# Optimization experiments

Hardware: AMD Instinct MI355X
Metric: run time of the kernel (lower is better)

Reference implementation:

```python
import jax, jax.numpy as jnp
import numpy as np

LAMBDA = 0.7
K = 3
HIDDEN = 8
IN_F = 512
OUT_F = 256
N = 4096


def _gat_layer(x, adj, W, a):
    # h = fc(x); e[i,j] = attn([h_i ; h_j]) = h_i @ a[:F] + h_j @ a[F:]
    # (same math as the N*N repeat/cat/linear, without materializing [N*N, 2F])
    h = x @ W                      # [N, F]
    F_ = h.shape[1]
    src = h @ a[:F_]               # [N, 1]
    dst = h @ a[F_:]               # [N, 1]
    e = src + dst.T                # [N, N]
    att = jax.nn.softmax(e, axis=1) * adj
    return jax.nn.elu(att @ h)     # [N, F]


def setup_inputs() -> dict:
    key = jax.random.key(0)
    ks = jax.random.split(key, 8)
    x = jax.random.normal(ks[0], (N, IN_F), dtype=jnp.float32)
    # binarized sparse-ish adjacency stored densely (avg degree ~41)
    adj = (jax.random.uniform(ks[1], (N, N)) < 0.01).astype(jnp.float32)
    W1 = jax.random.normal(ks[2], (IN_F, HIDDEN), dtype=jnp.float32) * (1.0 / np.sqrt(IN_F))
    a1 = jax.random.normal(ks[3], (2 * HIDDEN, 1), dtype=jnp.float32) * (1.0 / np.sqrt(2 * HIDDEN))
    W2 = jax.random.normal(ks[4], (HIDDEN, 1), dtype=jnp.float32) * (1.0 / np.sqrt(HIDDEN))
    a2 = jax.random.normal(ks[5], (2, 1), dtype=jnp.float32)
    W_sgc = jax.random.normal(ks[6], (IN_F * K, OUT_F), dtype=jnp.float32) * (1.0 / np.sqrt(IN_F * K))
    b_sgc = jnp.zeros((OUT_F,), dtype=jnp.float32)
    return {"x": x, "adj": adj, "W1": W1, "a1": a1, "W2": W2, "a2": a2,
            "W_sgc": W_sgc, "b_sgc": b_sgc}


def reference(x, adj, W1, a1, W2, a2, W_sgc, b_sgc):
    # GAT scoring head (dropout p=0.6 is identity at inference)
    h1 = _gat_layer(x, adj, W1, a1)
    node_scores = _gat_layer(h1, adj, W2, a2)        # [N, 1]

    # K-hop adjacency powers
    adj_list = [adj]
    for _ in range(1, K):
        adj_list.append(adj_list[-1] @ adj)

    # dynamic per-row masking (row-broadcast of node_scores > lambda)
    change_mask = (node_scores > LAMBDA).astype(adj.dtype)  # [N, 1] broadcasts over cols
    for k in range(K - 1):
        adj_list[k] = adj_list[k] * change_mask
        adj_list[k + 1] = adj_list[k + 1] * (1.0 - change_mask)

    # SGC: concat K hop-aggregated features, then linear
    agg = jnp.concatenate([A @ x for A in adj_list], axis=1)  # [N, K*IN_F]
    return agg @ W_sgc + b_sgc
```

## Files before the change

### kernel.cpp

```cpp
#include <hip/hip_runtime.h>
#include <hip/hip_bf16.h>
#include <cstddef>

#define NNODE 4096
#define INF   512
#define OUTF  256
#define HID   8
#define CAP   128

typedef __attribute__((ext_vector_type(8))) short short8;
typedef __attribute__((ext_vector_type(4))) float f32x4;

__device__ __forceinline__ unsigned short f2bf(float f){
  unsigned int u = __float_as_uint(f);
  u += 0x7fffu + ((u >> 16) & 1u);
  return (unsigned short)(u >> 16);
}

__global__ __launch_bounds__(256) void build_csr(const float* __restrict__ adj,
                                                 int* __restrict__ deg,
                                                 int* __restrict__ cols){
  int row = blockIdx.x, tid = threadIdx.x;
  __shared__ int cnt;
  if (tid == 0) cnt = 0;
  __syncthreads();
  const float4* arow = (const float4*)(adj + (size_t)row * NNODE);
  int* crow = cols + (size_t)row * CAP;
  #pragma unroll
  for (int k = 0; k < 4; k++){
    int idx = k * 256 + tid;
    float4 v = arow[idx];
    int n0 = (v.x != 0.f), n1 = (v.y != 0.f), n2 = (v.z != 0.f), n3 = (v.w != 0.f);
    int m = n0 + n1 + n2 + n3;
    if (m){
      int base = atomicAdd(&cnt, m);
      int c = idx * 4;
      if (n0){ if (base < CAP) crow[base] = c;     base++; }
      if (n1){ if (base < CAP) crow[base] = c + 1; base++; }
      if (n2){ if (base < CAP) crow[base] = c + 2; base++; }
      if (n3){ if (base < CAP) crow[base] = c + 3; }
    }
  }
  __syncthreads();
  if (tid == 0) deg[row] = cnt > CAP ? CAP : cnt;
}

__global__ __launch_bounds__(256) void gat_h(const float* __restrict__ x,
                                             const float* __restrict__ W1,
                                             const float* __restrict__ a1,
                                             float* __restrict__ h,
                                             float* __restrict__ dstv){
  int wave = threadIdx.x >> 6, lane = threadIdx.x & 63;
  int row = blockIdx.x * 4 + wave;
  const float* xr = x + (size_t)row * INF;
  float acc[HID];
  #pragma unroll
  for (int f = 0; f < HID; f++) acc[f] = 0.f;
  for (int k = lane; k < INF; k += 64){
    float xv = xr[k];
    const float* wp = W1 + (size_t)k * HID;
    #pragma unroll
    for (int f = 0; f < HID; f++) acc[f] += xv * wp[f];
  }
  #pragma unroll
  for (int f = 0; f < HID; f++)
    for (int o = 32; o >= 1; o >>= 1) acc[f] += __shfl_xor(acc[f], o, 64);
  if (lane == 0){
    float d = 0.f;
    #pragma unroll
    for (int f = 0; f < HID; f++){ h[(size_t)row*HID + f] = acc[f]; d += acc[f] * a1[HID + f]; }
    dstv[row] = d;
  }
}

__global__ __launch_bounds__(256) void gat_agg1_f(const float* __restrict__ h,
                                                  const float* __restrict__ dstv,
                                                  const int* __restrict__ deg,
                                                  const int* __restrict__ cols,
                                                  const float* __restrict__ W2,
                                                  float* __restrict__ h2){
  __shared__ float p[NNODE];
  __shared__ float red[4];
  int tid = threadIdx.x, lane = tid & 63, wv = tid >> 6;
  float mx = -INFINITY;
  for (int i = tid; i < NNODE; i += 256) mx = fmaxf(mx, dstv[i]);
  #pragma unroll
  for (int o = 32; o >= 1; o >>= 1) mx = fmaxf(mx, __shfl_xor(mx, o, 64));
  if (lane == 0) red[wv] = mx;
  __syncthreads();
  mx = fmaxf(fmaxf(red[0], red[1]), fmaxf(red[2], red[3]));
  __syncthreads();
  float sum = 0.f;
  for (int i = tid; i < NNODE; i += 256){ float e = expf(dstv[i] - mx); p[i] = e; sum += e; }
  #pragma unroll
  for (int o = 32; o >= 1; o >>= 1) sum += __shfl_xor(sum, o, 64);
  if (lane == 0) red[wv] = sum;
  __syncthreads();
  float inv = 1.0f / (red[0] + red[1] + red[2] + red[3]);
  for (int i = tid; i < NNODE; i += 256) p[i] *= inv;
  __syncthreads();

  int f = tid & 7, rg = tid >> 3;
  int row = blockIdx.x * 32 + rg;
  const int* cl = cols + (size_t)row * CAP;
  int d = deg[row];
  float acc = 0.f;
  for (int n = 0; n < d; n++){
    int j = cl[n];
    acc += p[j] * h[(size_t)j * HID + f];
  }
  float e = acc > 0.f ? acc : expm1f(acc);
  float t = e * W2[f];
  t += __shfl_xor(t, 1, 64);
  t += __shfl_xor(t, 2, 64);
  t += __shfl_xor(t, 4, 64);
  if (f == 0) h2[row] = t;
}

__global__ __launch_bounds__(256) void scores_mask_f(const float* __restrict__ h2,
                                                     const float* __restrict__ a2,
                                                     const int* __restrict__ deg,
                                                     const int* __restrict__ cols,
                                                     float* __restrict__ maskf){
  __shared__ float q[NNODE];
  __shared__ float red[4];
  int tid = threadIdx.x, lane = tid & 63, wv = tid >> 6;
  float s2 = a2[1];
  float mx = -INFINITY;
  for (int i = tid; i < NNODE; i += 256) mx = fmaxf(mx, s2 * h2[i]);
  #pragma unroll
  for (int o = 32; o >= 1; o >>= 1) mx = fmaxf(mx, __shfl_xor(mx, o, 64));
  if (lane == 0) red[wv] = mx;
  __syncthreads();
  mx = fmaxf(fmaxf(red[0], red[1]), fmaxf(red[2], red[3]));
  __syncthreads();
  float sum = 0.f;
  for (int i = tid; i < NNODE; i += 256){ float e = expf(s2 * h2[i] - mx); q[i] = e; sum += e; }
  #pragma unroll
  for (int o = 32; o >= 1; o >>= 1) sum += __shfl_xor(sum, o, 64);
  if (lane == 0) red[wv] = sum;
  __syncthreads();
  float inv = 1.0f / (red[0] + red[1] + red[2] + red[3]);
  for (int i = tid; i < NNODE; i += 256) q[i] = q[i] * inv * h2[i];
  __syncthreads();

  int row = blockIdx.x * 256 + tid;
  const int* cl = cols + (size_t)row * CAP;
  int d = deg[row];
  float s = 0.f;
  for (int n = 0; n < d; n++) s += q[cl[n]];
  float e = s > 0.f ? s : expm1f(s);
  maskf[row] = (e > 0.7f) ? 1.0f : 0.0f;
}

__global__ void convert_w(const float* __restrict__ Wsgc, unsigned short* __restrict__ wbT){
  int idx = blockIdx.x * 256 + threadIdx.x;
  if (idx >= 512 * 512) return;
  int c = idx >> 9, k = idx & 511;
  float val = (c < 256) ? Wsgc[(size_t)k * OUTF + c]
                        : Wsgc[(size_t)(1024 + k) * OUTF + (c - 256)];
  wbT[idx] = f2bf(val);
}

__global__ __launch_bounds__(256) void gemm_xw(const float* __restrict__ X,
                                               const unsigned short* __restrict__ BT,
                                               float* __restrict__ G){
  __shared__ unsigned short As[128][72];
  __shared__ unsigned short Bs[64][72];
  int tid = threadIdx.x;
  int wave = tid >> 6, lane = tid & 63;
  int row0 = blockIdx.x * 128;
  int col0 = blockIdx.y * 64;
  int wr = wave >> 1, wc = wave & 1;
  f32x4 acc[4][2];
  #pragma unroll
  for (int i = 0; i < 4; i++)
    #pragma unroll
    for (int j = 0; j < 2; j++)
      #pragma unroll
      for (int e = 0; e < 4; e++) acc[i][j][e] = 0.f;

  int mrow = lane & 15;
  int kq = (lane >> 4) * 8;

  for (int k0 = 0; k0 < 512; k0 += 64){
    #pragma unroll
    for (int ps = 0; ps < 4; ps++){
      int idx = ps * 256 + tid;
      int r = idx >> 3;
      int ko = (idx & 7) * 8;
      const float* src = X + ((size_t)(row0 + r) * 512 + k0 + ko);
      float4 v0 = ((const float4*)src)[0];
      float4 v1 = ((const float4*)src)[1];
      union { short8 v; unsigned short u[8]; } pk;
      pk.u[0] = f2bf(v0.x); pk.u[1] = f2bf(v0.y); pk.u[2] = f2bf(v0.z); pk.u[3] = f2bf(v0.w);
      pk.u[4] = f2bf(v1.x); pk.u[5] = f2bf(v1.y); pk.u[6] = f2bf(v1.z); pk.u[7] = f2bf(v1.w);
      *(short8*)(&As[r][ko]) = pk.v;
    }
    #pragma unroll
    for (int ps = 0; ps < 2; ps++){
      int idx = ps * 256 + tid;
      int c = idx >> 3;
      int ko = (idx & 7) * 8;
      int4 v = *(const int4*)(BT + ((size_t)(col0 + c) * 512 + k0 + ko));
      *(int4*)(&Bs[c][ko]) = v;
    }
    __syncthreads();
    #pragma unroll
    for (int kk = 0; kk < 2; kk++){
      short8 a[4], b[2];
      #pragma unroll
      for (int i = 0; i < 4; i++)
        a[i] = *(const short8*)(&As[wr * 64 + i * 16 + mrow][kk * 32 + kq]);
      #pragma unroll
      for (int j = 0; j < 2; j++)
        b[j] = *(const short8*)(&Bs[wc * 32 + j * 16 + mrow][kk * 32 + kq]);
      #pragma unroll
      for (int i = 0; i < 4; i++)
        #pragma unroll
        for (int j = 0; j < 2; j++)
          acc[i][j] = __builtin_amdgcn_mfma_f32_16x16x32_bf16(a[i], b[j], acc[i][j], 0, 0, 0);
    }
    __syncthreads();
  }
  int crow = (lane >> 4) * 4;
  int ccol = lane & 15;
  #pragma unroll
  for (int i = 0; i < 4; i++)
    #pragma unroll
    for (int j = 0; j < 2; j++)
      #pragma unroll
      for (int e = 0; e < 4; e++){
        int r = row0 + wr * 64 + i * 16 + crow + e;
        int c = col0 + wc * 32 + j * 16 + ccol;
        G[(size_t)r * 512 + c] = acc[i][j][e];
      }
}

__global__ __launch_bounds__(256) void hop4(const float* __restrict__ in, int instride,
                                            float* __restrict__ out,
                                            const int* __restrict__ deg,
                                            const int* __restrict__ cols){
  int wave = threadIdx.x >> 6, lane = threadIdx.x & 63;
  int row = blockIdx.x * 4 + wave;
  const int* cl = cols + (size_t)row * CAP;
  int d = deg[row];
  f32x4 acc = {0.f, 0.f, 0.f, 0.f};
  int n = 0;
  for (; n + 4 <= d; n += 4){
    int j0 = cl[n], j1 = cl[n+1], j2 = cl[n+2], j3 = cl[n+3];
    f32x4 a = ((const f32x4*)(in + (size_t)j0 * instride))[lane];
    f32x4 b = ((const f32x4*)(in + (size_t)j1 * instride))[lane];
    f32x4 c = ((const f32x4*)(in + (size_t)j2 * instride))[lane];
    f32x4 e = ((const f32x4*)(in + (size_t)j3 * instride))[lane];
    acc += a + b + c + e;
  }
  for (; n < d; n++)
    acc += ((const f32x4*)(in + (size_t)cl[n] * instride))[lane];
  ((f32x4*)(out + (size_t)row * OUTF))[lane] = acc;
}

__global__ __launch_bounds__(256) void hop_final(const float* __restrict__ Gleft,
                                                 const float* __restrict__ T2,
                                                 const float* __restrict__ maskf,
                                                 const float* __restrict__ b,
                                                 float* __restrict__ out,
                                                 const int* __restrict__ deg,
                                                 const int* __restrict__ cols){
  int wave = threadIdx.x >> 6, lane = threadIdx.x & 63;
  int row = blockIdx.x * 4 + wave;
  const int* cl = cols + (size_t)row * CAP;
  int d = deg[row];
  bool m = maskf[row] != 0.0f;
  const float* in = m ? Gleft : T2;
  int instride    = m ? 512   : 256;
  f32x4 acc = {0.f, 0.f, 0.f, 0.f};
  int n = 0;
  for (; n + 4 <= d; n += 4){
    int j0 = cl[n], j1 = cl[n+1], j2 = cl[n+2], j3 = cl[n+3];
    f32x4 a = ((const f32x4*)(in + (size_t)j0 * instride))[lane];
    f32x4 bb = ((const f32x4*)(in + (size_t)j1 * instride))[lane];
    f32x4 c = ((const f32x4*)(in + (size_t)j2 * instride))[lane];
    f32x4 e = ((const f32x4*)(in + (size_t)j3 * instride))[lane];
    acc += a + bb + c + e;
  }
  for (; n < d; n++)
    acc += ((const f32x4*)(in + (size_t)cl[n] * instride))[lane];
  f32x4 bias = ((const f32x4*)b)[lane];
  ((f32x4*)(out + (size_t)row * OUTF))[lane] = acc + bias;
}

extern "C" void kernel_launch(void* const* d_in, const int* in_sizes, int n_in,
                              void* d_out, int out_size, void* d_ws, size_t ws_size,
                              hipStream_t stream) {
  const float* x    = (const float*)d_in[0];
  const float* adj  = (const float*)d_in[1];
  const float* W1   = (const float*)d_in[2];
  const float* a1   = (const float*)d_in[3];
  const float* W2   = (const float*)d_in[4];
  const float* a2   = (const float*)d_in[5];
  const float* Wsgc = (const float*)d_in[6];
  const float* bsgc = (const float*)d_in[7];
  float* out = (float*)d_out;

  char* w = (char*)d_ws;
  size_t off = 0;
  auto carve = [&](size_t bytes) -> char* {
    char* p = w + off;
    off += (bytes + 255) & ~(size_t)255;
    return p;
  };
  int*   deg   = (int*)carve((size_t)NNODE * 4);
  int*   cols  = (int*)carve((size_t)NNODE * CAP * 4);
  float* h     = (float*)carve((size_t)NNODE * HID * 4);
  float* dstv  = (float*)carve((size_t)NNODE * 4);
  float* h2    = (float*)carve((size_t)NNODE * 4);
  float* maskf = (float*)carve((size_t)NNODE * 4);
  unsigned short* wbT = (unsigned short*)carve((size_t)512 * 512 * 2);
  float* G  = (float*)carve((size_t)NNODE * 512 * 4);
  float* T1 = (float*)carve((size_t)NNODE * OUTF * 4);
  float* T2 = (float*)carve((size_t)NNODE * OUTF * 4);

  build_csr<<<NNODE, 256, 0, stream>>>(adj, deg, cols);

  gat_h<<<NNODE / 4, 256, 0, stream>>>(x, W1, a1, h, dstv);
  gat_agg1_f<<<NNODE / 32, 256, 0, stream>>>(h, dstv, deg, cols, W2, h2);
  scores_mask_f<<<NNODE / 256, 256, 0, stream>>>(h2, a2, deg, cols, maskf);

  convert_w<<<1024, 256, 0, stream>>>(Wsgc, wbT);
  dim3 gg(32, 8);
  gemm_xw<<<gg, 256, 0, stream>>>(x, wbT, G);

  hop4<<<NNODE / 4, 256, 0, stream>>>(G + 256, 512, T1, deg, cols);
  hop4<<<NNODE / 4, 256, 0, stream>>>(T1, 256, T2, deg, cols);
  hop_final<<<NNODE / 4, 256, 0, stream>>>(G, T2, maskf, bsgc, out, deg, cols);
}
```

Baseline: 201.7 us.

## Fuse entire pipeline into one cooperative persistent kernel with bf16 intermediates

Replaces nine separate kernel launches with a single cooperative kernel of 256 blocks that uses grid.sync between phases. CSR build, GAT scoring, weight and x conversion, the MFMA GEMM and the three hop gathers now share one launch. The GAT softmax stages are overlapped with the hop gathers inside the same phase. Intermediates G, T1 and T2 are stored in bf16 to halve gather traffic, which adds rounding error in the hop results. The grid-wide barriers cost extra and each block recomputes the full softmax normalization.

```diff
diff --git a/kernel.cpp b/kernel.cpp
--- a/kernel.cpp
+++ b/kernel.cpp
@@ -1,12 +1,17 @@
 #include <hip/hip_runtime.h>
+#include <hip/hip_cooperative_groups.h>
 #include <hip/hip_bf16.h>
 #include <cstddef>
+
+namespace cg = cooperative_groups;
 
 #define NNODE 4096
 #define INF   512
 #define OUTF  256
 #define HID   8
 #define CAP   128
+#define NB    256
+#define NT    512
 
 typedef __attribute__((ext_vector_type(8))) short short8;
 typedef __attribute__((ext_vector_type(4))) float f32x4;
@@ -16,292 +21,298 @@
   u += 0x7fffu + ((u >> 16) & 1u);
   return (unsigned short)(u >> 16);
 }
-
-__global__ __launch_bounds__(256) void build_csr(const float* __restrict__ adj,
-                                                 int* __restrict__ deg,
-                                                 int* __restrict__ cols){
-  int row = blockIdx.x, tid = threadIdx.x;
-  __shared__ int cnt;
-  if (tid == 0) cnt = 0;
-  __syncthreads();
-  const float4* arow = (const float4*)(adj + (size_t)row * NNODE);
-  int* crow = cols + (size_t)row * CAP;
-  #pragma unroll
-  for (int k = 0; k < 4; k++){
-    int idx = k * 256 + tid;
-    float4 v = arow[idx];
-    int n0 = (v.x != 0.f), n1 = (v.y != 0.f), n2 = (v.z != 0.f), n3 = (v.w != 0.f);
-    int m = n0 + n1 + n2 + n3;
-    if (m){
-      int base = atomicAdd(&cnt, m);
-      int c = idx * 4;
-      if (n0){ if (base < CAP) crow[base] = c;     base++; }
-      if (n1){ if (base < CAP) crow[base] = c + 1; base++; }
-      if (n2){ if (base < CAP) crow[base] = c + 2; base++; }
-      if (n3){ if (base < CAP) crow[base] = c + 3; }
-    }
-  }
-  __syncthreads();
-  if (tid == 0) deg[row] = cnt > CAP ? CAP : cnt;
-}
-
-__global__ __launch_bounds__(256) void gat_h(const float* __restrict__ x,
-                                             const float* __restrict__ W1,
-                                             const float* __restrict__ a1,
-                                             float* __restrict__ h,
-                                             float* __restrict__ dstv){
-  int wave = threadIdx.x >> 6, lane = threadIdx.x & 63;
-  int row = blockIdx.x * 4 + wave;
-  const float* xr = x + (size_t)row * INF;
-  float acc[HID];
-  #pragma unroll
-  for (int f = 0; f < HID; f++) acc[f] = 0.f;
-  for (int k = lane; k < INF; k += 64){
-    float xv = xr[k];
-    const float* wp = W1 + (size_t)k * HID;
-    #pragma unroll
-    for (int f = 0; f < HID; f++) acc[f] += xv * wp[f];
-  }
-  #pragma unroll
-  for (int f = 0; f < HID; f++)
-    for (int o = 32; o >= 1; o >>= 1) acc[f] += __shfl_xor(acc[f], o, 64);
-  if (lane == 0){
-    float d = 0.f;
-    #pragma unroll
-    for (int f = 0; f < HID; f++){ h[(size_t)row*HID + f] = acc[f]; d += acc[f] * a1[HID + f]; }
-    dstv[row] = d;
-  }
-}
-
-__global__ __launch_bounds__(256) void gat_agg1_f(const float* __restrict__ h,
-                                                  const float* __restrict__ dstv,
-                                                  const int* __restrict__ deg,
-                                                  const int* __restrict__ cols,
-                                                  const float* __restrict__ W2,
-                                                  float* __restrict__ h2){
-  __shared__ float p[NNODE];
-  __shared__ float red[4];
-  int tid = threadIdx.x, lane = tid & 63, wv = tid >> 6;
-  float mx = -INFINITY;
-  for (int i = tid; i < NNODE; i += 256) mx = fmaxf(mx, dstv[i]);
-  #pragma unroll
-  for (int o = 32; o >= 1; o >>= 1) mx = fmaxf(mx, __shfl_xor(mx, o, 64));
-  if (lane == 0) red[wv] = mx;
-  __syncthreads();
-  mx = fmaxf(fmaxf(red[0], red[1]), fmaxf(red[2], red[3]));
-  __syncthreads();
-  float sum = 0.f;
-  for (int i = tid; i < NNODE; i += 256){ float e = expf(dstv[i] - mx); p[i] = e; sum += e; }
-  #pragma unroll
-  for (int o = 32; o >= 1; o >>= 1) sum += __shfl_xor(sum, o, 64);
-  if (lane == 0) red[wv] = sum;
-  __syncthreads();
-  float inv = 1.0f / (red[0] + red[1] + red[2] + red[3]);
-  for (int i = tid; i < NNODE; i += 256) p[i] *= inv;
-  __syncthreads();
-
-  int f = tid & 7, rg = tid >> 3;
-  int row = blockIdx.x * 32 + rg;
-  const int* cl = cols + (size_t)row * CAP;
-  int d = deg[row];
-  float acc = 0.f;
-  for (int n = 0; n < d; n++){
-    int j = cl[n];
-    acc += p[j] * h[(size_t)j * HID + f];
-  }
-  float e = acc > 0.f ? acc : expm1f(acc);
-  float t = e * W2[f];
-  t += __shfl_xor(t, 1, 64);
-  t += __shfl_xor(t, 2, 64);
-  t += __shfl_xor(t, 4, 64);
-  if (f == 0) h2[row] = t;
-}
-
-__global__ __launch_bounds__(256) void scores_mask_f(const float* __restrict__ h2,
-                                                     const float* __restrict__ a2,
-                                                     const int* __restrict__ deg,
-                                                     const int* __restrict__ cols,
-                                                     float* __restrict__ maskf){
-  __shared__ float q[NNODE];
-  __shared__ float red[4];
-  int tid = threadIdx.x, lane = tid & 63, wv = tid >> 6;
-  float s2 = a2[1];
-  float mx = -INFINITY;
-  for (int i = tid; i < NNODE; i += 256) mx = fmaxf(mx, s2 * h2[i]);
-  #pragma unroll
-  for (int o = 32; o >= 1; o >>= 1) mx = fmaxf(mx, __shfl_xor(mx, o, 64));
-  if (lane == 0) red[wv] = mx;
-  __syncthreads();
-  mx = fmaxf(fmaxf(red[0], red[1]), fmaxf(red[2], red[3]));
-  __syncthreads();
-  float sum = 0.f;
-  for (int i = tid; i < NNODE; i += 256){ float e = expf(s2 * h2[i] - mx); q[i] = e; sum += e; }
-  #pragma unroll
-  for (int o = 32; o >= 1; o >>= 1) sum += __shfl_xor(sum, o, 64);
-  if (lane == 0) red[wv] = sum;
-  __syncthreads();
-  float inv = 1.0f / (red[0] + red[1] + red[2] + red[3]);
-  for (int i = tid; i < NNODE; i += 256) q[i] = q[i] * inv * h2[i];
-  __syncthreads();
-
-  int row = blockIdx.x * 256 + tid;
-  const int* cl = cols + (size_t)row * CAP;
-  int d = deg[row];
-  float s = 0.f;
-  for (int n = 0; n < d; n++) s += q[cl[n]];
-  float e = s > 0.f ? s : expm1f(s);
-  maskf[row] = (e > 0.7f) ? 1.0f : 0.0f;
-}
-
-__global__ void convert_w(const float* __restrict__ Wsgc, unsigned short* __restrict__ wbT){
-  int idx = blockIdx.x * 256 + threadIdx.x;
-  if (idx >= 512 * 512) return;
-  int c = idx >> 9, k = idx & 511;
-  float val = (c < 256) ? Wsgc[(size_t)k * OUTF + c]
-                        : Wsgc[(size_t)(1024 + k) * OUTF + (c - 256)];
-  wbT[idx] = f2bf(val);
-}
-
-__global__ __launch_bounds__(256) void gemm_xw(const float* __restrict__ X,
-                                               const unsigned short* __restrict__ BT,
-                                               float* __restrict__ G){
-  __shared__ unsigned short As[128][72];
-  __shared__ unsigned short Bs[64][72];
-  int tid = threadIdx.x;
-  int wave = tid >> 6, lane = tid & 63;
-  int row0 = blockIdx.x * 128;
-  int col0 = blockIdx.y * 64;
-  int wr = wave >> 1, wc = wave & 1;
-  f32x4 acc[4][2];
-  #pragma unroll
-  for (int i = 0; i < 4; i++)
-    #pragma unroll
-    for (int j = 0; j < 2; j++)
-      #pragma unroll
-      for (int e = 0; e < 4; e++) acc[i][j][e] = 0.f;
-
-  int mrow = lane & 15;
-  int kq = (lane >> 4) * 8;
-
-  for (int k0 = 0; k0 < 512; k0 += 64){
-    #pragma unroll
-    for (int ps = 0; ps < 4; ps++){
-      int idx = ps * 256 + tid;
-      int r = idx >> 3;
-      int ko = (idx & 7) * 8;
-      const float* src = X + ((size_t)(row0 + r) * 512 + k0 + ko);
-      float4 v0 = ((const float4*)src)[0];
-      float4 v1 = ((const float4*)src)[1];
-      union { short8 v; unsigned short u[8]; } pk;
-      pk.u[0] = f2bf(v0.x); pk.u[1] = f2bf(v0.y); pk.u[2] = f2bf(v0.z); pk.u[3] = f2bf(v0.w);
-      pk.u[4] = f2bf(v1.x); pk.u[5] = f2bf(v1.y); pk.u[6] = f2bf(v1.z); pk.u[7] = f2bf(v1.w);
-      *(short8*)(&As[r][ko]) = pk.v;
-    }
-    #pragma unroll
-    for (int ps = 0; ps < 2; ps++){
-      int idx = ps * 256 + tid;
-      int c = idx >> 3;
-      int ko = (idx & 7) * 8;
-      int4 v = *(const int4*)(BT + ((size_t)(col0 + c) * 512 + k0 + ko));
-      *(int4*)(&Bs[c][ko]) = v;
-    }
-    __syncthreads();
-    #pragma unroll
-    for (int kk = 0; kk < 2; kk++){
-      short8 a[4], b[2];
-      #pragma unroll
-      for (int i = 0; i < 4; i++)
-        a[i] = *(const short8*)(&As[wr * 64 + i * 16 + mrow][kk * 32 + kq]);
-      #pragma unroll
-      for (int j = 0; j < 2; j++)
-        b[j] = *(const short8*)(&Bs[wc * 32 + j * 16 + mrow][kk * 32 + kq]);
-      #pragma unroll
-      for (int i = 0; i < 4; i++)
-        #pragma unroll
-        for (int j = 0; j < 2; j++)
-          acc[i][j] = __builtin_amdgcn_mfma_f32_16x16x32_bf16(a[i], b[j], acc[i][j], 0, 0, 0);
-    }
-    __syncthreads();
-  }
-  int crow = (lane >> 4) * 4;
-  int ccol = lane & 15;
-  #pragma unroll
-  for (int i = 0; i < 4; i++)
-    #pragma unroll
-    for (int j = 0; j < 2; j++)
-      #pragma unroll
-      for (int e = 0; e < 4; e++){
-        int r = row0 + wr * 64 + i * 16 + crow + e;
-        int c = col0 + wc * 32 + j * 16 + ccol;
-        G[(size_t)r * 512 + c] = acc[i][j][e];
-      }
-}
-
-__global__ __launch_bounds__(256) void hop4(const float* __restrict__ in, int instride,
-                                            float* __restrict__ out,
-                                            const int* __restrict__ deg,
-                                            const int* __restrict__ cols){
-  int wave = threadIdx.x >> 6, lane = threadIdx.x & 63;
-  int row = blockIdx.x * 4 + wave;
-  const int* cl = cols + (size_t)row * CAP;
-  int d = deg[row];
+__device__ __forceinline__ float bf2f(unsigned short s){
+  return __uint_as_float(((unsigned int)s) << 16);
+}
+
+struct KParams {
+  const float* x; const float* adj; const float* W1; const float* a1;
+  const float* W2; const float* a2; const float* Wsgc; const float* bsgc;
+  float* out;
+  int* deg; int* cols; float* h; float* dstv; float* h2; float* maskf;
+  unsigned short* xb; unsigned short* wbT; unsigned short* G;
+  unsigned short* T1; unsigned short* T2;
+};
+
+__device__ __forceinline__ f32x4 gather_row(const unsigned short* __restrict__ src,
+                                            int stride, const int* __restrict__ cl,
+                                            int d, int lane){
   f32x4 acc = {0.f, 0.f, 0.f, 0.f};
   int n = 0;
-  for (; n + 4 <= d; n += 4){
-    int j0 = cl[n], j1 = cl[n+1], j2 = cl[n+2], j3 = cl[n+3];
-    f32x4 a = ((const f32x4*)(in + (size_t)j0 * instride))[lane];
-    f32x4 b = ((const f32x4*)(in + (size_t)j1 * instride))[lane];
-    f32x4 c = ((const f32x4*)(in + (size_t)j2 * instride))[lane];
-    f32x4 e = ((const f32x4*)(in + (size_t)j3 * instride))[lane];
-    acc += a + b + c + e;
-  }
-  for (; n < d; n++)
-    acc += ((const f32x4*)(in + (size_t)cl[n] * instride))[lane];
-  ((f32x4*)(out + (size_t)row * OUTF))[lane] = acc;
-}
-
-__global__ __launch_bounds__(256) void hop_final(const float* __restrict__ Gleft,
-                                                 const float* __restrict__ T2,
-                                                 const float* __restrict__ maskf,
-                                                 const float* __restrict__ b,
-                                                 float* __restrict__ out,
-                                                 const int* __restrict__ deg,
-                                                 const int* __restrict__ cols){
-  int wave = threadIdx.x >> 6, lane = threadIdx.x & 63;
-  int row = blockIdx.x * 4 + wave;
-  const int* cl = cols + (size_t)row * CAP;
-  int d = deg[row];
-  bool m = maskf[row] != 0.0f;
-  const float* in = m ? Gleft : T2;
-  int instride    = m ? 512   : 256;
-  f32x4 acc = {0.f, 0.f, 0.f, 0.f};
-  int n = 0;
-  for (; n + 4 <= d; n += 4){
-    int j0 = cl[n], j1 = cl[n+1], j2 = cl[n+2], j3 = cl[n+3];
-    f32x4 a = ((const f32x4*)(in + (size_t)j0 * instride))[lane];
-    f32x4 bb = ((const f32x4*)(in + (size_t)j1 * instride))[lane];
-    f32x4 c = ((const f32x4*)(in + (size_t)j2 * instride))[lane];
-    f32x4 e = ((const f32x4*)(in + (size_t)j3 * instride))[lane];
-    acc += a + bb + c + e;
-  }
-  for (; n < d; n++)
-    acc += ((const f32x4*)(in + (size_t)cl[n] * instride))[lane];
-  f32x4 bias = ((const f32x4*)b)[lane];
-  ((f32x4*)(out + (size_t)row * OUTF))[lane] = acc + bias;
+  for (; n + 8 <= d; n += 8){
+    ushort4 v[8];
+    #pragma unroll
+    for (int u = 0; u < 8; u++){
+      int j = cl[n + u];
+      v[u] = *(const ushort4*)(src + (size_t)j * stride + lane * 4);
+    }
+    #pragma unroll
+    for (int u = 0; u < 8; u++){
+      acc[0] += bf2f(v[u].x); acc[1] += bf2f(v[u].y);
+      acc[2] += bf2f(v[u].z); acc[3] += bf2f(v[u].w);
+    }
+  }
+  for (; n < d; n++){
+    int j = cl[n];
+    ushort4 vv = *(const ushort4*)(src + (size_t)j * stride + lane * 4);
+    acc[0] += bf2f(vv.x); acc[1] += bf2f(vv.y); acc[2] += bf2f(vv.z); acc[3] += bf2f(vv.w);
+  }
+  return acc;
+}
+
+__device__ __forceinline__ void store_bf4(unsigned short* dst, f32x4 a){
+  union { ushort4 v; unsigned short u[4]; } o;
+  o.u[0] = f2bf(a[0]); o.u[1] = f2bf(a[1]); o.u[2] = f2bf(a[2]); o.u[3] = f2bf(a[3]);
+  *(ushort4*)dst = o.v;
+}
+
+__global__ __launch_bounds__(NT, 2) void fused_all(KParams P){
+  cg::grid_group grid = cg::this_grid();
+  __shared__ __align__(16) char smem[27648];
+  __shared__ float red[8];
+  __shared__ int cnts[16];
+  const int tid = threadIdx.x, lane = tid & 63, wv = tid >> 6;
+  const int b = blockIdx.x, rowBase = b * 16;
+
+  if (tid < 16) cnts[tid] = 0;
+  __syncthreads();
+
+  #pragma unroll
+  for (int t = 0; t < 2; t++){
+    int e = t * (NB * NT) + b * NT + tid;
+    int c = e >> 9, k = e & 511;
+    float val = (c < OUTF) ? P.Wsgc[(size_t)k * OUTF + c]
+                           : P.Wsgc[(size_t)(1024 + k) * OUTF + (c - OUTF)];
+    P.wbT[e] = f2bf(val);
+  }
+  #pragma unroll
+  for (int t = 0; t < 2; t++){
+    int g = t * NT + tid;
+    int r = g >> 6, ko = (g & 63) * 8;
+    const float* src = P.x + (size_t)(rowBase + r) * INF + ko;
+    float4 v0 = ((const float4*)src)[0];
+    float4 v1 = ((const float4*)src)[1];
+    union { short8 v; unsigned short u[8]; } pk;
+    pk.u[0]=f2bf(v0.x); pk.u[1]=f2bf(v0.y); pk.u[2]=f2bf(v0.z); pk.u[3]=f2bf(v0.w);
+    pk.u[4]=f2bf(v1.x); pk.u[5]=f2bf(v1.y); pk.u[6]=f2bf(v1.z); pk.u[7]=f2bf(v1.w);
+    *(short8*)(P.xb + (size_t)(rowBase + r) * INF + ko) = pk.v;
+  }
+  for (int rr = 0; rr < 2; rr++){
+    int row = rowBase + wv * 2 + rr;
+    const float* xr = P.x + (size_t)row * INF;
+    float acc[HID];
+    #pragma unroll
+    for (int f = 0; f < HID; f++) acc[f] = 0.f;
+    for (int k = lane; k < INF; k += 64){
+      float xv = xr[k];
+      const float* wp = P.W1 + (size_t)k * HID;
+      #pragma unroll
+      for (int f = 0; f < HID; f++) acc[f] += xv * wp[f];
+    }
+    #pragma unroll
+    for (int f = 0; f < HID; f++)
+      for (int o = 32; o >= 1; o >>= 1) acc[f] += __shfl_xor(acc[f], o, 64);
+    if (lane == 0){
+      float d = 0.f;
+      #pragma unroll
+      for (int f = 0; f < HID; f++){ P.h[(size_t)row*HID + f] = acc[f]; d += acc[f] * P.a1[HID + f]; }
+      P.dstv[row] = d;
+    }
+  }
+  for (int rr = 0; rr < 2; rr++){
+    int lrow = wv * 2 + rr, row = rowBase + lrow;
+    const float4* arow = (const float4*)(P.adj + (size_t)row * NNODE);
+    int* crow = P.cols + (size_t)row * CAP;
+    for (int kk = 0; kk < 16; kk++){
+      int idx = kk * 64 + lane;
+      float4 v = arow[idx];
+      int n0=(v.x!=0.f), n1=(v.y!=0.f), n2=(v.z!=0.f), n3=(v.w!=0.f);
+      int m = n0 + n1 + n2 + n3;
+      if (m){
+        int base = atomicAdd(&cnts[lrow], m);
+        int c = idx * 4;
+        if (n0){ if (base < CAP) crow[base] = c;     base++; }
+        if (n1){ if (base < CAP) crow[base] = c + 1; base++; }
+        if (n2){ if (base < CAP) crow[base] = c + 2; base++; }
+        if (n3){ if (base < CAP) crow[base] = c + 3; }
+      }
+    }
+  }
+  __syncthreads();
+  if (tid < 16) P.deg[rowBase + tid] = cnts[tid] > CAP ? CAP : cnts[tid];
+  grid.sync();
+
+  {
+    unsigned short (*As)[72] = (unsigned short (*)[72])smem;
+    unsigned short (*Bs)[72] = (unsigned short (*)[72])(smem + 128*72*2);
+    int row0 = (b >> 3) * 128;
+    int col0 = (b & 7) * 64;
+    int wr = wv >> 1, wc = wv & 1;
+    f32x4 acc[2][2];
+    #pragma unroll
+    for (int i = 0; i < 2; i++)
+      #pragma unroll
+      for (int j = 0; j < 2; j++)
+        #pragma unroll
+        for (int e = 0; e < 4; e++) acc[i][j][e] = 0.f;
+    int mrow = lane & 15;
+    int kq = (lane >> 4) * 8;
+    for (int k0 = 0; k0 < 512; k0 += 64){
+      #pragma unroll
+      for (int t = 0; t < 2; t++){
+        int id = t * NT + tid;
+        int r = id >> 3, ko = (id & 7) * 8;
+        *(int4*)(&As[r][ko]) = *(const int4*)(P.xb + (size_t)(row0 + r) * 512 + k0 + ko);
+      }
+      { int c = tid >> 3, ko = (tid & 7) * 8;
+        *(int4*)(&Bs[c][ko]) = *(const int4*)(P.wbT + (size_t)(col0 + c) * 512 + k0 + ko); }
+      __syncthreads();
+      #pragma unroll
+      for (int kk = 0; kk < 2; kk++){
+        short8 a0 = *(const short8*)(&As[wr*32 +  0 + mrow][kk*32 + kq]);
+        short8 a1 = *(const short8*)(&As[wr*32 + 16 + mrow][kk*32 + kq]);
+        short8 b0 = *(const short8*)(&Bs[wc*32 +  0 + mrow][kk*32 + kq]);
+        short8 b1 = *(const short8*)(&Bs[wc*32 + 16 + mrow][kk*32 + kq]);
+        acc[0][0] = __builtin_amdgcn_mfma_f32_16x16x32_bf16(a0, b0, acc[0][0], 0, 0, 0);
+        acc[0][1] = __builtin_amdgcn_mfma_f32_16x16x32_bf16(a0, b1, acc[0][1], 0, 0, 0);
+        acc[1][0] = __builtin_amdgcn_mfma_f32_16x16x32_bf16(a1, b0, acc[1][0], 0, 0, 0);
+        acc[1][1] = __builtin_amdgcn_mfma_f32_16x16x32_bf16(a1, b1, acc[1][1], 0, 0, 0);
+      }
+      __syncthreads();
+    }
+    int crow = (lane >> 4) * 4, ccol = lane & 15;
+    #pragma unroll
+    for (int i = 0; i < 2; i++)
+      #pragma unroll
+      for (int j = 0; j < 2; j++)
+        #pragma unroll
+        for (int e = 0; e < 4; e++){
+          int r = row0 + wr*32 + i*16 + crow + e;
+          int c = col0 + wc*32 + j*16 + ccol;
+          P.G[(size_t)r * 512 + c] = f2bf(acc[i][j][e]);
+        }
+  }
+  grid.sync();
+
+  {
+    float* pb = (float*)smem;
+    float mx = -INFINITY;
+    for (int i = tid; i < NNODE; i += NT) mx = fmaxf(mx, P.dstv[i]);
+    #pragma unroll
+    for (int o = 32; o >= 1; o >>= 1) mx = fmaxf(mx, __shfl_xor(mx, o, 64));
+    if (lane == 0) red[wv] = mx;
+    __syncthreads();
+    mx = red[0];
+    #pragma unroll
+    for (int i = 1; i < 8; i++) mx = fmaxf(mx, red[i]);
+    __syncthreads();
+    float sum = 0.f;
+    for (int i = tid; i < NNODE; i += NT){ float e = expf(P.dstv[i] - mx); pb[i] = e; sum += e; }
+    #pragma unroll
+    for (int o = 32; o >= 1; o >>= 1) sum += __shfl_xor(sum, o, 64);
+    if (lane == 0) red[wv] = sum;
+    __syncthreads();
+    float tot = 0.f;
+    #pragma unroll
+    for (int i = 0; i < 8; i++) tot += red[i];
+    float inv = 1.0f / tot;
+    for (int i = tid; i < NNODE; i += NT) pb[i] *= inv;
+    __syncthreads();
+
+    if (tid < 128){
+      int f = tid & 7, rg = tid >> 3;
+      int row = rowBase + rg;
+      const int* cl = P.cols + (size_t)row * CAP;
+      int d = P.deg[row];
+      float a = 0.f;
+      for (int n = 0; n < d; n++){
+        int j = cl[n];
+        a += pb[j] * P.h[(size_t)j * HID + f];
+      }
+      float e = a > 0.f ? a : expm1f(a);
+      float t = e * P.W2[f];
+      t += __shfl_xor(t, 1, 64);
+      t += __shfl_xor(t, 2, 64);
+      t += __shfl_xor(t, 4, 64);
+      if (f == 0) P.h2[row] = t;
+    }
+    for (int rr = 0; rr < 2; rr++){
+      int row = rowBase + wv * 2 + rr;
+      f32x4 a = gather_row(P.G + 256, 512, P.cols + (size_t)row * CAP, P.deg[row], lane);
+      store_bf4(P.T1 + (size_t)row * 256 + lane * 4, a);
+    }
+  }
+  grid.sync();
+
+  {
+    float* pb = (float*)smem;
+    float s2 = P.a2[1];
+    float mx = -INFINITY;
+    for (int i = tid; i < NNODE; i += NT) mx = fmaxf(mx, s2 * P.h2[i]);
+    #pragma unroll
+    for (int o = 32; o >= 1; o >>= 1) mx = fmaxf(mx, __shfl_xor(mx, o, 64));
+    if (lane == 0) red[wv] = mx;
+    __syncthreads();
+    mx = red[0];
+    #pragma unroll
+    for (int i = 1; i < 8; i++) mx = fmaxf(mx, red[i]);
+    __syncthreads();
+    float sum = 0.f;
+    for (int i = tid; i < NNODE; i += NT){ float e = expf(s2 * P.h2[i] - mx); pb[i] = e; sum += e; }
+    #pragma unroll
+    for (int o = 32; o >= 1; o >>= 1) sum += __shfl_xor(sum, o, 64);
+    if (lane == 0) red[wv] = sum;
+    __syncthreads();
+    float tot = 0.f;
+    #pragma unroll
+    for (int i = 0; i < 8; i++) tot += red[i];
+    float inv = 1.0f / tot;
+    for (int i = tid; i < NNODE; i += NT) pb[i] = pb[i] * inv * P.h2[i];
+    __syncthreads();
+
+    if (tid < 16){
+      int row = rowBase + tid;
+      const int* cl = P.cols + (size_t)row * CAP;
+      int d = P.deg[row];
+      float s = 0.f;
+      for (int n = 0; n < d; n++) s += pb[cl[n]];
+      float e = s > 0.f ? s : expm1f(s);
+      P.maskf[row] = (e > 0.7f) ? 1.0f : 0.0f;
+    }
+    for (int rr = 0; rr < 2; rr++){
+      int row = rowBase + wv * 2 + rr;
+      f32x4 a = gather_row(P.T1, 256, P.cols + (size_t)row * CAP, P.deg[row], lane);
+      store_bf4(P.T2 + (size_t)row * 256 + lane * 4, a);
+    }
+  }
+  grid.sync();
+
+  for (int rr = 0; rr < 2; rr++){
+    int row = rowBase + wv * 2 + rr;
+    bool m = P.maskf[row] != 0.0f;
+    const unsigned short* src = m ? P.G : P.T2;
+    int stride = m ? 512 : 256;
+    f32x4 a = gather_row(src, stride, P.cols + (size_t)row * CAP, P.deg[row], lane);
+    float4 bias = ((const float4*)P.bsgc)[lane];
+    float4 o;
+    o.x = a[0] + bias.x; o.y = a[1] + bias.y; o.z = a[2] + bias.z; o.w = a[3] + bias.w;
+    ((float4*)(P.out + (size_t)row * OUTF))[lane] = o;
+  }
 }
 
 extern "C" void kernel_launch(void* const* d_in, const int* in_sizes, int n_in,
                               void* d_out, int out_size, void* d_ws, size_t ws_size,
                               hipStream_t stream) {
-  const float* x    = (const float*)d_in[0];
-  const float* adj  = (const float*)d_in[1];
-  const float* W1   = (const float*)d_in[2];
-  const float* a1   = (const float*)d_in[3];
-  const float* W2   = (const float*)d_in[4];
-  const float* a2   = (const float*)d_in[5];
-  const float* Wsgc = (const float*)d_in[6];
-  const float* bsgc = (const float*)d_in[7];
-  float* out = (float*)d_out;
+  KParams P;
+  P.x    = (const float*)d_in[0];
+  P.adj  = (const float*)d_in[1];
+  P.W1   = (const float*)d_in[2];
+  P.a1   = (const float*)d_in[3];
+  P.W2   = (const float*)d_in[4];
+  P.a2   = (const float*)d_in[5];
+  P.Wsgc = (const float*)d_in[6];
+  P.bsgc = (const float*)d_in[7];
+  P.out  = (float*)d_out;
 
   char* w = (char*)d_ws;
   size_t off = 0;
@@ -310,28 +321,18 @@
     off += (bytes + 255) & ~(size_t)255;
     return p;
   };
-  int*   deg   = (int*)carve((size_t)NNODE * 4);
-  int*   cols  = (int*)carve((size_t)NNODE * CAP * 4);
-  float* h     = (float*)carve((size_t)NNODE * HID * 4);
-  float* dstv  = (float*)carve((size_t)NNODE * 4);
-  float* h2    = (float*)carve((size_t)NNODE * 4);
-  float* maskf = (float*)carve((size_t)NNODE * 4);
-  unsigned short* wbT = (unsigned short*)carve((size_t)512 * 512 * 2);
-  float* G  = (float*)carve((size_t)NNODE * 512 * 4);
-  float* T1 = (float*)carve((size_t)NNODE * OUTF * 4);
-  float* T2 = (float*)carve((size_t)NNODE * OUTF * 4);
-
-  build_csr<<<NNODE, 256, 0, stream>>>(adj, deg, cols);
-
-  gat_h<<<NNODE / 4, 256, 0, stream>>>(x, W1, a1, h, dstv);
-  gat_agg1_f<<<NNODE / 32, 256, 0, stream>>>(h, dstv, deg, cols, W2, h2);
-  scores_mask_f<<<NNODE / 256, 256, 0, stream>>>(h2, a2, deg, cols, maskf);
-
-  convert_w<<<1024, 256, 0, stream>>>(Wsgc, wbT);
-  dim3 gg(32, 8);
-  gemm_xw<<<gg, 256, 0, stream>>>(x, wbT, G);
-
-  hop4<<<NNODE / 4, 256, 0, stream>>>(G + 256, 512, T1, deg, cols);
-  hop4<<<NNODE / 4, 256, 0, stream>>>(T1, 256, T2, deg, cols);
-  hop_final<<<NNODE / 4, 256, 0, stream>>>(G, T2, maskf, bsgc, out, deg, cols);
-}
+  P.deg   = (int*)carve((size_t)NNODE * 4);
+  P.cols  = (int*)carve((size_t)NNODE * CAP * 4);
+  P.h     = (float*)carve((size_t)NNODE * HID * 4);
+  P.dstv  = (float*)carve((size_t)NNODE * 4);
+  P.h2    = (float*)carve((size_t)NNODE * 4);
+  P.maskf = (float*)carve((size_t)NNODE * 4);
+  P.xb    = (unsigned short*)carve((size_t)NNODE * INF * 2);
+  P.wbT   = (unsigned short*)carve((size_t)512 * 512 * 2);
+  P.G     = (unsigned short*)carve((size_t)NNODE * 512 * 2);
+  P.T1    = (unsigned short*)carve((size_t)NNODE * OUTF * 2);
+  P.T2    = (unsigned short*)carve((size_t)NNODE * OUTF * 2);
+
+  void* args[] = { &P };
+  hipLaunchCooperativeKernel((const void*)fused_all, dim3(NB), dim3(NT), args, 0, stream);
+}
```

New measurement: 327.4 us. 62.3% more time.
